# Kernel tuning notes

Measured on AMD Instinct MI355X. Metric: run time of the kernel, lower is better.

## Reference

```python
import jax, jax.numpy as jnp
import numpy as np

N_NODES = 50000
N_EDGES = 600000
BAG = 16
VOCAB = 10000
EMB = 128
HID = 128
N_CLASSES = 10
N_GRAPHS = 512
PAD_IDX = 1


def setup_inputs() -> dict:
    key = jax.random.key(0)
    ks = jax.random.split(key, 12)
    x_tokens = jax.random.randint(ks[0], (N_NODES, BAG), 0, VOCAB)
    src = jax.random.randint(ks[1], (N_EDGES,), 0, N_NODES)
    dst = jax.random.randint(ks[2], (N_EDGES,), 0, N_NODES)
    edge_index = jnp.stack([src, dst])
    batch = jnp.sort(jax.random.randint(ks[3], (N_NODES,), 0, N_GRAPHS))
    # rows 0,1 are zero in the original (weights[2:] filled from pretrained vectors)
    emb_table = (jax.random.normal(ks[4], (VOCAB, EMB)) * 0.02).at[:2].set(0.0)
    s = 1.0 / np.sqrt(EMB)
    w1_l = jax.random.normal(ks[5], (HID, EMB)) * s
    b1 = jnp.zeros((HID,), jnp.float32)
    w1_r = jax.random.normal(ks[6], (HID, EMB)) * s
    w2_l = jax.random.normal(ks[7], (HID, HID)) * s
    b2 = jnp.zeros((HID,), jnp.float32)
    w2_r = jax.random.normal(ks[8], (HID, HID)) * s
    w_out = jax.random.normal(ks[9], (N_CLASSES, HID)) * s
    b_out = jnp.zeros((N_CLASSES,), jnp.float32)
    return {"x_tokens": x_tokens, "edge_index": edge_index, "batch": batch,
            "emb_table": emb_table, "w1_l": w1_l, "b1": b1, "w1_r": w1_r,
            "w2_l": w2_l, "b2": b2, "w2_r": w2_r, "w_out": w_out, "b_out": b_out}


def _embedding_bag_mean(tokens, table):
    # nn.EmbeddingBag mode='mean' with padding_idx: padding tokens excluded from mean
    emb = table[tokens]                                  # [N, BAG, D]
    mask = (tokens != PAD_IDX)[..., None].astype(table.dtype)
    total = jnp.sum(emb * mask, axis=1)                  # [N, D]
    cnt = jnp.clip(jnp.sum(mask, axis=1), 1.0)           # [N, 1]
    return total / cnt


def _sage_conv(x, src, dst, w_l, b_l, w_r):
    # PyG SAGEConv: lin_l(mean_{j in N(i)} x_j) + lin_r(x_i); lin_r has no bias
    n = x.shape[0]
    msg_sum = jax.ops.segment_sum(x[src], dst, num_segments=n)           # [N, D]
    deg = jax.ops.segment_sum(jnp.ones((src.shape[0], 1), x.dtype), dst,
                              num_segments=n)                             # [N, 1]
    aggr = msg_sum / jnp.clip(deg, 1.0)
    return aggr @ w_l.T + b_l + x @ w_r.T


def reference(x_tokens, edge_index, batch, emb_table, w1_l, b1, w1_r,
              w2_l, b2, w2_r, w_out, b_out):
    src, dst = edge_index[0], edge_index[1]
    x = _embedding_bag_mean(x_tokens, emb_table)                 # [N, EMB]
    x = jax.nn.relu(_sage_conv(x, src, dst, w1_l, b1, w1_r))     # [N, HID]
    x = jax.nn.relu(_sage_conv(x, src, dst, w2_l, b2, w2_r))     # [N, HID]
    # global_mean_pool over graph ids
    g_sum = jax.ops.segment_sum(x, batch, num_segments=N_GRAPHS)
    g_cnt = jax.ops.segment_sum(jnp.ones((x.shape[0], 1), x.dtype), batch,
                                num_segments=N_GRAPHS)
    g = g_sum / jnp.clip(g_cnt, 1.0)                             # [G, HID]
    return g @ w_out.T + b_out                                   # [G, C]
```

## Files before the change

kernel.cpp:

```cpp
#include <hip/hip_runtime.h>
#include <hip/hip_bf16.h>

#define NN 50000
#define NE 600000
#define BAG 16
#define EMB 128
#define HID 128
#define NC 10
#define NG 512
#define PAD_IDX 1
#define VOCAB 10000
#define SLOTS 64
#define TPAIRS (VOCAB * EMB / 2)
#define WPAIRS (4 * HID * EMB / 2)
#define EMVB (NN / 16)
#define NCH1 293
#define RANGES 125
#define RNODES 400
#define QCAP 6400
#define NTILES ((NN + 127) / 128)

typedef __attribute__((ext_vector_type(8))) short v8s;
typedef __attribute__((ext_vector_type(4))) float v4f;

__device__ __forceinline__ float bflo(unsigned u) { return __uint_as_float(u << 16); }
__device__ __forceinline__ float bfhi(unsigned u) { return __uint_as_float(u & 0xffff0000u); }
__device__ __forceinline__ unsigned short f2bf(float f) {
    unsigned u = __float_as_uint(f);
    return (unsigned short)((u + 0x7fffu + ((u >> 16) & 1u)) >> 16);
}
__device__ __forceinline__ void acc8(float* a, v8s v) {
    unsigned* u = (unsigned*)&v;
#pragma unroll
    for (int j = 0; j < 4; j++) {
        a[2 * j] += bflo(u[j]);
        a[2 * j + 1] += bfhi(u[j]);
    }
}

__global__ void k_conv(const float* __restrict__ t, unsigned short* __restrict__ tb,
                       const float* __restrict__ w1l, const float* __restrict__ w1r,
                       const float* __restrict__ w2l, const float* __restrict__ w2r,
                       unsigned short* __restrict__ wbf, int* __restrict__ qtail,
                       float* __restrict__ gsum, float* __restrict__ gcnt,
                       unsigned short* __restrict__ x0, unsigned short* __restrict__ x1) {
    int i = blockIdx.x * blockDim.x + threadIdx.x;
    if (i < RANGES) qtail[i] = 0;
    if (i < NG * HID) gsum[i] = 0.f;
    if (i < NG) gcnt[i] = 0.f;
    if (i < 64) {
        ((unsigned*)(x0 + (size_t)NN * EMB))[i] = 0;
        ((unsigned*)(x1 + (size_t)NN * HID))[i] = 0;
    }
    if (i < TPAIRS) {
        float2 v = *(const float2*)(t + (size_t)i * 2);
        unsigned lo = f2bf(v.x), hi = f2bf(v.y);
        *(unsigned*)(tb + (size_t)i * 2) = lo | (hi << 16);
    } else if (i < TPAIRS + WPAIRS) {
        int j = i - TPAIRS;
        int k = j * 2;
        int arr = k >> 14;
        int o = k & 16383;
        const float* w = (arr == 0) ? w1l : (arr == 1) ? w1r : (arr == 2) ? w2l : w2r;
        float2 v = *(const float2*)(w + o);
        unsigned lo = f2bf(v.x), hi = f2bf(v.y);
        *(unsigned*)(wbf + k) = lo | (hi << 16);
    }
}

__global__ __launch_bounds__(256) void k_scatem(const int* __restrict__ src,
                                                const int* __restrict__ dst,
                                                int* __restrict__ qtail,
                                                unsigned* __restrict__ queue,
                                                const int* __restrict__ tokens,
                                                const unsigned short* __restrict__ table,
                                                unsigned short* __restrict__ x0) {
    __shared__ int qcntL[RANGES];
    __shared__ unsigned qbufL[RANGES * 64];
    int b = blockIdx.x;
    int tid = threadIdx.x;

    if (b < NCH1) {
        for (int i = tid; i < RANGES; i += 256) qcntL[i] = 0;
        __syncthreads();
        int e0 = b * 2048 + tid * 8;
        if (e0 < NE) {
            int4 s0 = *((const int4*)(src + e0));
            int4 s1 = *((const int4*)(src + e0) + 1);
            int4 d0 = *((const int4*)(dst + e0));
            int4 d1 = *((const int4*)(dst + e0) + 1);
            int ss[8] = {s0.x, s0.y, s0.z, s0.w, s1.x, s1.y, s1.z, s1.w};
            int dd[8] = {d0.x, d0.y, d0.z, d0.w, d1.x, d1.y, d1.z, d1.w};
#pragma unroll
            for (int j = 0; j < 8; j++) {
                int q = dd[j] / RNODES;
                unsigned pk = ((unsigned)(dd[j] - q * RNODES) << 16) | (unsigned)ss[j];
                int pos = atomicAdd(&qcntL[q], 1);
                if (pos < 64) qbufL[q * 64 + pos] = pk;
            }
        }
        __syncthreads();
        if (tid < RANGES) {
            int n = qcntL[tid];
            if (n > 64) n = 64;
            int base = atomicAdd(&qtail[tid], n);
            if (base + n > QCAP) n = (QCAP - base > 0) ? QCAP - base : 0;
            unsigned* qp = queue + (size_t)tid * QCAP + base;
            for (int k = 0; k < n; k++) qp[k] = qbufL[tid * 64 + k];
        }
        return;
    }

    int sl = tid & 15;
    int node = (b - NCH1) * 16 + (tid >> 4);
    const int* tp = tokens + node * BAG;
    int tk[16];
    *(int4*)(tk) = *(const int4*)(tp);
    *(int4*)(tk + 4) = *(const int4*)(tp + 4);
    *(int4*)(tk + 8) = *(const int4*)(tp + 8);
    *(int4*)(tk + 12) = *(const int4*)(tp + 12);
    int c = 0;
#pragma unroll
    for (int t = 0; t < BAG; t++) c += (tk[t] != PAD_IDX);
    float a[8];
#pragma unroll
    for (int j = 0; j < 8; j++) a[j] = 0.f;
#pragma unroll
    for (int h = 0; h < 2; h++) {
        v8s v[8];
#pragma unroll
        for (int t = 0; t < 8; t++)
            v[t] = *(const v8s*)(table + (size_t)tk[h * 8 + t] * EMB + sl * 8);
#pragma unroll
        for (int t = 0; t < 8; t++) acc8(a, v[t]);
    }
    float inv = 1.0f / (float)(c > 0 ? c : 1);
    uint4 o;
    o.x = f2bf(a[0] * inv) | ((unsigned)f2bf(a[1] * inv) << 16);
    o.y = f2bf(a[2] * inv) | ((unsigned)f2bf(a[3] * inv) << 16);
    o.z = f2bf(a[4] * inv) | ((unsigned)f2bf(a[5] * inv) << 16);
    o.w = f2bf(a[6] * inv) | ((unsigned)f2bf(a[7] * inv) << 16);
    *(uint4*)(x0 + (size_t)node * EMB + sl * 8) = o;
}

__global__ __launch_bounds__(256) void k_csr(const int* __restrict__ qtail,
                                             const unsigned* __restrict__ queue,
                                             int* __restrict__ cnt,
                                             unsigned short* __restrict__ slots) {
    __shared__ int cntL[RNODES];
    __shared__ __align__(16) unsigned short slotsL[RNODES * SLOTS];
    int r = blockIdx.x, tid = threadIdx.x;
    for (int i = tid; i < RNODES; i += 256) cntL[i] = 0;
    __syncthreads();
    int n = qtail[r];
    if (n > QCAP) n = QCAP;
    const unsigned* qp = queue + (size_t)r * QCAP;
    for (int i = tid; i < n; i += 256) {
        unsigned u = qp[i];
        int dl = u >> 16;
        int p = atomicAdd(&cntL[dl], 1);
        if (p < SLOTS) slotsL[dl * SLOTS + p] = (unsigned short)(u & 0xffffu);
    }
    __syncthreads();
    for (int i = tid; i < RNODES; i += 256) {
        int d = cntL[i];
        if (d > SLOTS) d = SLOTS;
        int d8 = (d + 7) & ~7;
        if (d8 > SLOTS) d8 = SLOTS;
        for (int p = d; p < d8; p++) slotsL[i * SLOTS + p] = (unsigned short)NN;
    }
    __syncthreads();
    uint4* gs = (uint4*)(slots + (size_t)r * RNODES * SLOTS);
    const uint4* ls = (const uint4*)slotsL;
    for (int i = tid; i < RNODES * SLOTS / 8; i += 256) gs[i] = ls[i];
    for (int i = tid; i < RNODES; i += 256) cnt[r * RNODES + i] = cntL[i];
}

__global__ __launch_bounds__(256) void k_aggr(const unsigned short* __restrict__ x,
                                              const int* __restrict__ cnt,
                                              const unsigned short* __restrict__ slots,
                                              unsigned short* __restrict__ aggr) {
    int wv = threadIdx.x >> 6;
    int lane = threadIdx.x & 63;
    int n0 = (blockIdx.x * 4 + wv) * 2;
    int n1 = n0 + 1;
    int g = lane >> 4, sl = lane & 15;
    int deg0 = cnt[n0], deg1 = cnt[n1];
    int m0 = deg0 > SLOTS ? SLOTS : deg0;
    int m1 = deg1 > SLOTS ? SLOTS : deg1;
    int m80 = (m0 + 7) & ~7;
    int m81 = (m1 + 7) & ~7;
    int idx0 = slots[(size_t)n0 * SLOTS + lane];
    int idx1 = slots[(size_t)n1 * SLOTS + lane];
    float a0[8], a1[8];
#pragma unroll
    for (int j = 0; j < 8; j++) {
        a0[j] = 0.f;
        a1[j] = 0.f;
    }
    int mm = m80 > m81 ? m80 : m81;
#pragma unroll 2
    for (int i = 0; i < mm; i += 8) {
        bool c0 = (i < m80), c1 = (i < m81);
        v8s w0, w1, w2, w3;
        if (c0) {
            int t00 = __shfl(idx0, i + g, 64);
            int t01 = __shfl(idx0, i + 4 + g, 64);
            w0 = *(const v8s*)(x + (size_t)t00 * HID + sl * 8);
            w1 = *(const v8s*)(x + (size_t)t01 * HID + sl * 8);
        }
        if (c1) {
            int t10 = __shfl(idx1, i + g, 64);
            int t11 = __shfl(idx1, i + 4 + g, 64);
            w2 = *(const v8s*)(x + (size_t)t10 * HID + sl * 8);
            w3 = *(const v8s*)(x + (size_t)t11 * HID + sl * 8);
        }
        if (c0) {
            acc8(a0, w0);
            acc8(a0, w1);
        }
        if (c1) {
            acc8(a1, w2);
            acc8(a1, w3);
        }
    }
#pragma unroll
    for (int j = 0; j < 8; j++) {
        a0[j] += __shfl_xor(a0[j], 16, 64);
        a0[j] += __shfl_xor(a0[j], 32, 64);
        a1[j] += __shfl_xor(a1[j], 16, 64);
        a1[j] += __shfl_xor(a1[j], 32, 64);
    }
    if (g == 0) {
        float inv = 1.0f / (float)(deg0 > 0 ? deg0 : 1);
        uint4 o;
        o.x = f2bf(a0[0] * inv) | ((unsigned)f2bf(a0[1] * inv) << 16);
        o.y = f2bf(a0[2] * inv) | ((unsigned)f2bf(a0[3] * inv) << 16);
        o.z = f2bf(a0[4] * inv) | ((unsigned)f2bf(a0[5] * inv) << 16);
        o.w = f2bf(a0[6] * inv) | ((unsigned)f2bf(a0[7] * inv) << 16);
        *(uint4*)(aggr + (size_t)n0 * HID + sl * 8) = o;
    } else if (g == 1) {
        float inv = 1.0f / (float)(deg1 > 0 ? deg1 : 1);
        uint4 o;
        o.x = f2bf(a1[0] * inv) | ((unsigned)f2bf(a1[1] * inv) << 16);
        o.y = f2bf(a1[2] * inv) | ((unsigned)f2bf(a1[3] * inv) << 16);
        o.z = f2bf(a1[4] * inv) | ((unsigned)f2bf(a1[5] * inv) << 16);
        o.w = f2bf(a1[6] * inv) | ((unsigned)f2bf(a1[7] * inv) << 16);
        *(uint4*)(aggr + (size_t)n1 * HID + sl * 8) = o;
    }
}

__device__ __forceinline__ void sage_kloop(int row0, const unsigned short* __restrict__ xa,
                                           const unsigned short* __restrict__ xr,
                                           const unsigned short* __restrict__ wl,
                                           const unsigned short* __restrict__ wr,
                                           unsigned short* As, unsigned short* Bs,
                                           v4f acc[2][8]) {
    int tid = threadIdx.x;
    int wave = tid >> 6, lane = tid & 63;
    int q = lane >> 4, l16 = lane & 15;
    for (int kc = 0; kc < 8; kc++) {
        const unsigned short* Ag = (kc < 4) ? xa : xr;
        const unsigned short* Bg = (kc < 4) ? wl : wr;
        int koff = (kc & 3) * 32;
#pragma unroll
        for (int it = 0; it < 2; it++) {
            int seg = tid + it * 256;
            int r = seg >> 2, sg = seg & 3;
            int gr = row0 + r;
            if (gr > NN - 1) gr = NN - 1;
            v8s a = *(const v8s*)(Ag + (size_t)gr * HID + koff + sg * 8);
            *(v8s*)(As + r * 32 + sg * 8) = a;
            v8s b = *(const v8s*)(Bg + (size_t)r * HID + koff + sg * 8);
            *(v8s*)(Bs + r * 32 + sg * 8) = b;
        }
        __syncthreads();
        v8s a0 = *(const v8s*)(As + (wave * 32 + l16) * 32 + q * 8);
        v8s a1 = *(const v8s*)(As + (wave * 32 + 16 + l16) * 32 + q * 8);
#pragma unroll
        for (int nt = 0; nt < 8; nt++) {
            v8s b = *(const v8s*)(Bs + (nt * 16 + l16) * 32 + q * 8);
            acc[0][nt] = __builtin_amdgcn_mfma_f32_16x16x32_bf16(a0, b, acc[0][nt], 0, 0, 0);
            acc[1][nt] = __builtin_amdgcn_mfma_f32_16x16x32_bf16(a1, b, acc[1][nt], 0, 0, 0);
        }
        __syncthreads();
    }
}

__global__ __launch_bounds__(256) void k_sage(const unsigned short* __restrict__ xa,
                                              const unsigned short* __restrict__ xr,
                                              const unsigned short* __restrict__ wl,
                                              const unsigned short* __restrict__ wr,
                                              const float* __restrict__ bias,
                                              unsigned short* __restrict__ out) {
    __shared__ unsigned short As[128 * 32];
    __shared__ unsigned short Bs[128 * 32];
    int row0 = blockIdx.x * 128;
    v4f acc[2][8];
#pragma unroll
    for (int m = 0; m < 2; m++)
#pragma unroll
        for (int n = 0; n < 8; n++) acc[m][n] = (v4f){0.f, 0.f, 0.f, 0.f};
    sage_kloop(row0, xa, xr, wl, wr, As, Bs, acc);
    int tid = threadIdx.x;
    int wave = tid >> 6, lane = tid & 63;
    int q = lane >> 4, l16 = lane & 15;
#pragma unroll
    for (int nt = 0; nt < 8; nt++) {
        int col = nt * 16 + l16;
        float bv = bias[col];
#pragma unroll
        for (int mt = 0; mt < 2; mt++) {
#pragma unroll
            for (int r = 0; r < 4; r++) {
                int row = row0 + wave * 32 + mt * 16 + q * 4 + r;
                if (row < NN) {
                    float v = acc[mt][nt][r] + bv;
                    v = v > 0.f ? v : 0.f;
                    out[(size_t)row * HID + col] = f2bf(v);
                }
            }
        }
    }
}

__global__ __launch_bounds__(256) void k_sagepool(const unsigned short* __restrict__ xa,
                                                  const unsigned short* __restrict__ xr,
                                                  const unsigned short* __restrict__ wl,
                                                  const unsigned short* __restrict__ wr,
                                                  const float* __restrict__ bias,
                                                  const int* __restrict__ batch,
                                                  float* __restrict__ gsum,
                                                  float* __restrict__ gcnt) {
    __shared__ unsigned short smem[128 * 128];
    unsigned short* As = smem;
    unsigned short* Bs = smem + 128 * 32;
    int row0 = blockIdx.x * 128;
    v4f acc[2][8];
#pragma unroll
    for (int m = 0; m < 2; m++)
#pragma unroll
        for (int n = 0; n < 8; n++) acc[m][n] = (v4f){0.f, 0.f, 0.f, 0.f};
    sage_kloop(row0, xa, xr, wl, wr, As, Bs, acc);
    int tid = threadIdx.x;
    int wave = tid >> 6, lane = tid & 63;
    int q = lane >> 4, l16 = lane & 15;
#pragma unroll
    for (int nt = 0; nt < 8; nt++) {
        int col = nt * 16 + l16;
        float bv = bias[col];
#pragma unroll
        for (int mt = 0; mt < 2; mt++) {
#pragma unroll
            for (int r = 0; r < 4; r++) {
                int rl = wave * 32 + mt * 16 + q * 4 + r;
                float v = acc[mt][nt][r] + bv;
                v = v > 0.f ? v : 0.f;
                smem[rl * 128 + col] = f2bf(v);
            }
        }
    }
    __syncthreads();
    if (tid < 128) {
        int col = tid;
        int end = NN - row0;
        if (end > 128) end = 128;
        int cur = batch[row0];
        float acc_p = 0.f;
        int c = 0;
        for (int i = 0; i < end; i++) {
            int b = batch[row0 + i];
            if (b != cur) {
                atomicAdd(&gsum[cur * HID + col], acc_p);
                if (col == 0) atomicAdd(&gcnt[cur], (float)c);
                acc_p = 0.f;
                c = 0;
                cur = b;
            }
            acc_p += __uint_as_float(((unsigned)smem[i * 128 + col]) << 16);
            c++;
        }
        atomicAdd(&gsum[cur * HID + col], acc_p);
        if (col == 0) atomicAdd(&gcnt[cur], (float)c);
    }
}

__global__ __launch_bounds__(128) void k_final(const float* __restrict__ gsum,
                                               const float* __restrict__ gcnt,
                                               const float* __restrict__ w_out,
                                               const float* __restrict__ b_out,
                                               float* __restrict__ out) {
    __shared__ float mean[HID];
    int g = blockIdx.x, tid = threadIdx.x;
    mean[tid] = gsum[g * HID + tid] / fmaxf(gcnt[g], 1.0f);
    __syncthreads();
    if (tid < NC) {
        float s = b_out[tid];
#pragma unroll 16
        for (int d = 0; d < HID; d++) s += mean[d] * w_out[tid * HID + d];
        out[g * NC + tid] = s;
    }
}

extern "C" void kernel_launch(void* const* d_in, const int* in_sizes, int n_in,
                              void* d_out, int out_size, void* d_ws, size_t ws_size,
                              hipStream_t stream) {
    const int* x_tokens = (const int*)d_in[0];
    const int* edge = (const int*)d_in[1];
    const int* batch = (const int*)d_in[2];
    const float* emb_table = (const float*)d_in[3];
    const float* w1l = (const float*)d_in[4];
    const float* b1 = (const float*)d_in[5];
    const float* w1r = (const float*)d_in[6];
    const float* w2l = (const float*)d_in[7];
    const float* b2 = (const float*)d_in[8];
    const float* w2r = (const float*)d_in[9];
    const float* w_out = (const float*)d_in[10];
    const float* b_out = (const float*)d_in[11];
    float* out = (float*)d_out;

    char* ws = (char*)d_ws;
    size_t off = 0;
    auto alloc = [&](size_t bytes) {
        void* p = ws + off;
        off += (bytes + 255) & ~(size_t)255;
        return p;
    };
    int* cnt = (int*)alloc(NN * 4);
    unsigned short* slots = (unsigned short*)alloc((size_t)NN * SLOTS * 2);
    unsigned short* wbf = (unsigned short*)alloc(4 * HID * EMB * 2);
    float* gsum = (float*)alloc(NG * HID * 4);
    float* gcnt = (float*)alloc(NG * 4);
    unsigned short* x0 = (unsigned short*)alloc((size_t)(NN + 1) * EMB * 2);
    unsigned short* x1 = (unsigned short*)alloc((size_t)(NN + 1) * HID * 2);
    unsigned short* aggrb = (unsigned short*)alloc((size_t)NN * HID * 2);
    unsigned* queue = (unsigned*)alloc((size_t)RANGES * QCAP * 4);
    int* qtail = (int*)alloc(RANGES * 4);
    unsigned short* table_bf = x1;

    const int* srcp = edge;
    const int* dstp = edge + NE;

    k_conv<<<(TPAIRS + WPAIRS + 255) / 256, 256, 0, stream>>>(
        emb_table, table_bf, w1l, w1r, w2l, w2r, wbf, qtail, gsum, gcnt, x0, x1);
    k_scatem<<<NCH1 + EMVB, 256, 0, stream>>>(srcp, dstp, qtail, queue, x_tokens,
                                              table_bf, x0);
    k_csr<<<RANGES, 256, 0, stream>>>(qtail, queue, cnt, slots);
    k_aggr<<<NN / 8, 256, 0, stream>>>(x0, cnt, slots, aggrb);
    k_sage<<<NTILES, 256, 0, stream>>>(aggrb, x0, wbf, wbf + 16384, b1, x1);
    k_aggr<<<NN / 8, 256, 0, stream>>>(x1, cnt, slots, aggrb);
    k_sagepool<<<NTILES, 256, 0, stream>>>(aggrb, x1, wbf + 32768, wbf + 49152, b2,
                                           batch, gsum, gcnt);
    k_final<<<NG, 128, 0, stream>>>(gsum, gcnt, w_out, b_out, out);
}
```

Baseline: 198.0 us.

## Fuse edge bucketing into conversion kernel and CSR into embed kernel; pipeline GEMM loads

```diff
diff --git a/kernel.cpp b/kernel.cpp
--- a/kernel.cpp
+++ b/kernel.cpp
@@ -13,12 +13,14 @@
 #define SLOTS 64
 #define TPAIRS (VOCAB * EMB / 2)
 #define WPAIRS (4 * HID * EMB / 2)
-#define EMVB (NN / 16)
+#define CONVB ((TPAIRS + WPAIRS + 255) / 256)
 #define NCH1 293
 #define RANGES 125
 #define RNODES 400
-#define QCAP 6400
+#define CSRB (RANGES * 2)
+#define EMVB (NN / 16)
 #define NTILES ((NN + 127) / 128)
+#define ASTR 40
 
 typedef __attribute__((ext_vector_type(8))) short v8s;
 typedef __attribute__((ext_vector_type(4))) float v4f;
@@ -38,14 +40,55 @@
     }
 }
 
-__global__ void k_conv(const float* __restrict__ t, unsigned short* __restrict__ tb,
-                       const float* __restrict__ w1l, const float* __restrict__ w1r,
-                       const float* __restrict__ w2l, const float* __restrict__ w2r,
-                       unsigned short* __restrict__ wbf, int* __restrict__ qtail,
-                       float* __restrict__ gsum, float* __restrict__ gcnt,
-                       unsigned short* __restrict__ x0, unsigned short* __restrict__ x1) {
-    int i = blockIdx.x * blockDim.x + threadIdx.x;
-    if (i < RANGES) qtail[i] = 0;
+__global__ __launch_bounds__(256) void k_conv(const int* __restrict__ src,
+                                              const int* __restrict__ dst,
+                                              unsigned* __restrict__ queue,
+                                              int* __restrict__ qcntG,
+                                              const float* __restrict__ t,
+                                              unsigned short* __restrict__ tb,
+                                              const float* __restrict__ w1l,
+                                              const float* __restrict__ w1r,
+                                              const float* __restrict__ w2l,
+                                              const float* __restrict__ w2r,
+                                              unsigned short* __restrict__ wbf,
+                                              float* __restrict__ gsum,
+                                              float* __restrict__ gcnt,
+                                              unsigned short* __restrict__ x0,
+                                              unsigned short* __restrict__ x1) {
+    __shared__ int qcL[RANGES];
+    __shared__ unsigned qbL[RANGES * 64];
+    int b = blockIdx.x;
+    int tid = threadIdx.x;
+    if (b < NCH1) {
+        for (int i = tid; i < RANGES; i += 256) qcL[i] = 0;
+        __syncthreads();
+        int e0 = b * 2048 + tid * 8;
+        if (e0 < NE) {
+            int4 s0 = *((const int4*)(src + e0));
+            int4 s1 = *((const int4*)(src + e0) + 1);
+            int4 d0 = *((const int4*)(dst + e0));
+            int4 d1 = *((const int4*)(dst + e0) + 1);
+            int ss[8] = {s0.x, s0.y, s0.z, s0.w, s1.x, s1.y, s1.z, s1.w};
+            int dd[8] = {d0.x, d0.y, d0.z, d0.w, d1.x, d1.y, d1.z, d1.w};
+#pragma unroll
+            for (int j = 0; j < 8; j++) {
+                int q = dd[j] / RNODES;
+                unsigned pk = ((unsigned)(dd[j] - q * RNODES) << 16) | (unsigned)ss[j];
+                int pos = atomicAdd(&qcL[q], 1);
+                if (pos < 64) qbL[q * 64 + pos] = pk;
+            }
+        }
+        __syncthreads();
+        if (tid < RANGES) {
+            int n = qcL[tid];
+            if (n > 64) n = 64;
+            qcntG[tid * NCH1 + b] = n;
+            unsigned* qp = queue + ((size_t)tid * NCH1 + b) * 64;
+            for (int k = 0; k < n; k++) qp[k] = qbL[tid * 64 + k];
+        }
+        return;
+    }
+    int i = (b - NCH1) * 256 + tid;
     if (i < NG * HID) gsum[i] = 0.f;
     if (i < NG) gcnt[i] = 0.f;
     if (i < 64) {
@@ -68,51 +111,52 @@
     }
 }
 
-__global__ __launch_bounds__(256) void k_scatem(const int* __restrict__ src,
-                                                const int* __restrict__ dst,
-                                                int* __restrict__ qtail,
-                                                unsigned* __restrict__ queue,
+__global__ __launch_bounds__(256) void k_scatem(const int* __restrict__ qcntG,
+                                                const unsigned* __restrict__ queue,
+                                                int* __restrict__ cnt,
+                                                unsigned short* __restrict__ slots,
                                                 const int* __restrict__ tokens,
                                                 const unsigned short* __restrict__ table,
                                                 unsigned short* __restrict__ x0) {
-    __shared__ int qcntL[RANGES];
-    __shared__ unsigned qbufL[RANGES * 64];
+    __shared__ int cntL[200];
+    __shared__ __align__(16) unsigned short slotsL[200 * SLOTS];
     int b = blockIdx.x;
     int tid = threadIdx.x;
-
-    if (b < NCH1) {
-        for (int i = tid; i < RANGES; i += 256) qcntL[i] = 0;
-        __syncthreads();
-        int e0 = b * 2048 + tid * 8;
-        if (e0 < NE) {
-            int4 s0 = *((const int4*)(src + e0));
-            int4 s1 = *((const int4*)(src + e0) + 1);
-            int4 d0 = *((const int4*)(dst + e0));
-            int4 d1 = *((const int4*)(dst + e0) + 1);
-            int ss[8] = {s0.x, s0.y, s0.z, s0.w, s1.x, s1.y, s1.z, s1.w};
-            int dd[8] = {d0.x, d0.y, d0.z, d0.w, d1.x, d1.y, d1.z, d1.w};
-#pragma unroll
-            for (int j = 0; j < 8; j++) {
-                int q = dd[j] / RNODES;
-                unsigned pk = ((unsigned)(dd[j] - q * RNODES) << 16) | (unsigned)ss[j];
-                int pos = atomicAdd(&qcntL[q], 1);
-                if (pos < 64) qbufL[q * 64 + pos] = pk;
+    if (b < CSRB) {
+        int r = b >> 1, half = b & 1;
+        for (int i = tid; i < 200; i += 256) cntL[i] = 0;
+        __syncthreads();
+        int dlo = half * 200;
+        for (int c = tid; c < NCH1; c += 256) {
+            int n = qcntG[r * NCH1 + c];
+            const unsigned* qp = queue + ((size_t)r * NCH1 + c) * 64;
+            for (int k = 0; k < n; k++) {
+                unsigned u = qp[k];
+                int d2 = (int)(u >> 16) - dlo;
+                if ((unsigned)d2 < 200u) {
+                    int p = atomicAdd(&cntL[d2], 1);
+                    if (p < SLOTS) slotsL[d2 * SLOTS + p] = (unsigned short)(u & 0xffffu);
+                }
             }
         }
         __syncthreads();
-        if (tid < RANGES) {
-            int n = qcntL[tid];
-            if (n > 64) n = 64;
-            int base = atomicAdd(&qtail[tid], n);
-            if (base + n > QCAP) n = (QCAP - base > 0) ? QCAP - base : 0;
-            unsigned* qp = queue + (size_t)tid * QCAP + base;
-            for (int k = 0; k < n; k++) qp[k] = qbufL[tid * 64 + k];
-        }
+        for (int i = tid; i < 200; i += 256) {
+            int d = cntL[i];
+            if (d > SLOTS) d = SLOTS;
+            int d8 = (d + 7) & ~7;
+            if (d8 > SLOTS) d8 = SLOTS;
+            for (int p = d; p < d8; p++) slotsL[i * SLOTS + p] = (unsigned short)NN;
+        }
+        __syncthreads();
+        int nb = r * RNODES + half * 200;
+        uint4* gs = (uint4*)(slots + (size_t)nb * SLOTS);
+        const uint4* ls = (const uint4*)slotsL;
+        for (int i = tid; i < 200 * SLOTS / 8; i += 256) gs[i] = ls[i];
+        for (int i = tid; i < 200; i += 256) cnt[nb + i] = cntL[i];
         return;
     }
-
     int sl = tid & 15;
-    int node = (b - NCH1) * 16 + (tid >> 4);
+    int node = (b - CSRB) * 16 + (tid >> 4);
     const int* tp = tokens + node * BAG;
     int tk[16];
     *(int4*)(tk) = *(const int4*)(tp);
@@ -125,15 +169,12 @@
     float a[8];
 #pragma unroll
     for (int j = 0; j < 8; j++) a[j] = 0.f;
-#pragma unroll
-    for (int h = 0; h < 2; h++) {
-        v8s v[8];
-#pragma unroll
-        for (int t = 0; t < 8; t++)
-            v[t] = *(const v8s*)(table + (size_t)tk[h * 8 + t] * EMB + sl * 8);
-#pragma unroll
-        for (int t = 0; t < 8; t++) acc8(a, v[t]);
-    }
+    v8s v[16];
+#pragma unroll
+    for (int t = 0; t < 16; t++)
+        v[t] = *(const v8s*)(table + (size_t)tk[t] * EMB + sl * 8);
+#pragma unroll
+    for (int t = 0; t < 16; t++) acc8(a, v[t]);
     float inv = 1.0f / (float)(c > 0 ? c : 1);
     uint4 o;
     o.x = f2bf(a[0] * inv) | ((unsigned)f2bf(a[1] * inv) << 16);
@@ -141,39 +182,6 @@
     o.z = f2bf(a[4] * inv) | ((unsigned)f2bf(a[5] * inv) << 16);
     o.w = f2bf(a[6] * inv) | ((unsigned)f2bf(a[7] * inv) << 16);
     *(uint4*)(x0 + (size_t)node * EMB + sl * 8) = o;
-}
-
-__global__ __launch_bounds__(256) void k_csr(const int* __restrict__ qtail,
-                                             const unsigned* __restrict__ queue,
-                                             int* __restrict__ cnt,
-                                             unsigned short* __restrict__ slots) {
-    __shared__ int cntL[RNODES];
-    __shared__ __align__(16) unsigned short slotsL[RNODES * SLOTS];
-    int r = blockIdx.x, tid = threadIdx.x;
-    for (int i = tid; i < RNODES; i += 256) cntL[i] = 0;
-    __syncthreads();
-    int n = qtail[r];
-    if (n > QCAP) n = QCAP;
-    const unsigned* qp = queue + (size_t)r * QCAP;
-    for (int i = tid; i < n; i += 256) {
-        unsigned u = qp[i];
-        int dl = u >> 16;
-        int p = atomicAdd(&cntL[dl], 1);
-        if (p < SLOTS) slotsL[dl * SLOTS + p] = (unsigned short)(u & 0xffffu);
-    }
-    __syncthreads();
-    for (int i = tid; i < RNODES; i += 256) {
-        int d = cntL[i];
-        if (d > SLOTS) d = SLOTS;
-        int d8 = (d + 7) & ~7;
-        if (d8 > SLOTS) d8 = SLOTS;
-        for (int p = d; p < d8; p++) slotsL[i * SLOTS + p] = (unsigned short)NN;
-    }
-    __syncthreads();
-    uint4* gs = (uint4*)(slots + (size_t)r * RNODES * SLOTS);
-    const uint4* ls = (const uint4*)slotsL;
-    for (int i = tid; i < RNODES * SLOTS / 8; i += 256) gs[i] = ls[i];
-    for (int i = tid; i < RNODES; i += 256) cnt[r * RNODES + i] = cntL[i];
 }
 
 __global__ __launch_bounds__(256) void k_aggr(const unsigned short* __restrict__ x,
@@ -259,32 +267,43 @@
     int tid = threadIdx.x;
     int wave = tid >> 6, lane = tid & 63;
     int q = lane >> 4, l16 = lane & 15;
+    int r0 = tid >> 2, sg = tid & 3;
+    int r1 = (tid + 256) >> 2;
+    int gr0 = row0 + r0;
+    if (gr0 > NN - 1) gr0 = NN - 1;
+    int gr1 = row0 + r1;
+    if (gr1 > NN - 1) gr1 = NN - 1;
+    v8s ra0 = *(const v8s*)(xa + (size_t)gr0 * HID + sg * 8);
+    v8s ra1 = *(const v8s*)(xa + (size_t)gr1 * HID + sg * 8);
+    v8s rb0 = *(const v8s*)(wl + (size_t)r0 * HID + sg * 8);
+    v8s rb1 = *(const v8s*)(wl + (size_t)r1 * HID + sg * 8);
     for (int kc = 0; kc < 8; kc++) {
-        const unsigned short* Ag = (kc < 4) ? xa : xr;
-        const unsigned short* Bg = (kc < 4) ? wl : wr;
-        int koff = (kc & 3) * 32;
-#pragma unroll
-        for (int it = 0; it < 2; it++) {
-            int seg = tid + it * 256;
-            int r = seg >> 2, sg = seg & 3;
-            int gr = row0 + r;
-            if (gr > NN - 1) gr = NN - 1;
-            v8s a = *(const v8s*)(Ag + (size_t)gr * HID + koff + sg * 8);
-            *(v8s*)(As + r * 32 + sg * 8) = a;
-            v8s b = *(const v8s*)(Bg + (size_t)r * HID + koff + sg * 8);
-            *(v8s*)(Bs + r * 32 + sg * 8) = b;
-        }
-        __syncthreads();
-        v8s a0 = *(const v8s*)(As + (wave * 32 + l16) * 32 + q * 8);
-        v8s a1 = *(const v8s*)(As + (wave * 32 + 16 + l16) * 32 + q * 8);
+        __syncthreads();
+        *(v8s*)(As + r0 * ASTR + sg * 8) = ra0;
+        *(v8s*)(As + r1 * ASTR + sg * 8) = ra1;
+        *(v8s*)(Bs + r0 * ASTR + sg * 8) = rb0;
+        *(v8s*)(Bs + r1 * ASTR + sg * 8) = rb1;
+        __syncthreads();
+        if (kc < 7) {
+            int kn = kc + 1;
+            const unsigned short* Ag = (kn < 4) ? xa : xr;
+            const unsigned short* Bg = (kn < 4) ? wl : wr;
+            int koff = (kn & 3) * 32;
+            ra0 = *(const v8s*)(Ag + (size_t)gr0 * HID + koff + sg * 8);
+            ra1 = *(const v8s*)(Ag + (size_t)gr1 * HID + koff + sg * 8);
+            rb0 = *(const v8s*)(Bg + (size_t)r0 * HID + koff + sg * 8);
+            rb1 = *(const v8s*)(Bg + (size_t)r1 * HID + koff + sg * 8);
+        }
+        v8s a0 = *(const v8s*)(As + (wave * 32 + l16) * ASTR + q * 8);
+        v8s a1 = *(const v8s*)(As + (wave * 32 + 16 + l16) * ASTR + q * 8);
 #pragma unroll
         for (int nt = 0; nt < 8; nt++) {
-            v8s b = *(const v8s*)(Bs + (nt * 16 + l16) * 32 + q * 8);
+            v8s b = *(const v8s*)(Bs + (nt * 16 + l16) * ASTR + q * 8);
             acc[0][nt] = __builtin_amdgcn_mfma_f32_16x16x32_bf16(a0, b, acc[0][nt], 0, 0, 0);
             acc[1][nt] = __builtin_amdgcn_mfma_f32_16x16x32_bf16(a1, b, acc[1][nt], 0, 0, 0);
         }
-        __syncthreads();
-    }
+    }
+    __syncthreads();
 }
 
 __global__ __launch_bounds__(256) void k_sage(const unsigned short* __restrict__ xa,
@@ -293,8 +312,8 @@
                                               const unsigned short* __restrict__ wr,
                                               const float* __restrict__ bias,
                                               unsigned short* __restrict__ out) {
-    __shared__ unsigned short As[128 * 32];
-    __shared__ unsigned short Bs[128 * 32];
+    __shared__ unsigned short As[128 * ASTR];
+    __shared__ unsigned short Bs[128 * ASTR];
     int row0 = blockIdx.x * 128;
     v4f acc[2][8];
 #pragma unroll
@@ -334,7 +353,7 @@
                                                   float* __restrict__ gcnt) {
     __shared__ unsigned short smem[128 * 128];
     unsigned short* As = smem;
-    unsigned short* Bs = smem + 128 * 32;
+    unsigned short* Bs = smem + 128 * ASTR;
     int row0 = blockIdx.x * 128;
     v4f acc[2][8];
 #pragma unroll
@@ -434,18 +453,18 @@
     unsigned short* x0 = (unsigned short*)alloc((size_t)(NN + 1) * EMB * 2);
     unsigned short* x1 = (unsigned short*)alloc((size_t)(NN + 1) * HID * 2);
     unsigned short* aggrb = (unsigned short*)alloc((size_t)NN * HID * 2);
-    unsigned* queue = (unsigned*)alloc((size_t)RANGES * QCAP * 4);
-    int* qtail = (int*)alloc(RANGES * 4);
+    unsigned* queue = (unsigned*)alloc((size_t)RANGES * NCH1 * 64 * 4);
+    int* qcntG = (int*)alloc((size_t)RANGES * NCH1 * 4);
     unsigned short* table_bf = x1;
 
     const int* srcp = edge;
     const int* dstp = edge + NE;
 
-    k_conv<<<(TPAIRS + WPAIRS + 255) / 256, 256, 0, stream>>>(
-        emb_table, table_bf, w1l, w1r, w2l, w2r, wbf, qtail, gsum, gcnt, x0, x1);
-    k_scatem<<<NCH1 + EMVB, 256, 0, stream>>>(srcp, dstp, qtail, queue, x_tokens,
+    k_conv<<<NCH1 + CONVB, 256, 0, stream>>>(srcp, dstp, queue, qcntG, emb_table,
+                                             table_bf, w1l, w1r, w2l, w2r, wbf,
+                                             gsum, gcnt, x0, x1);
+    k_scatem<<<CSRB + EMVB, 256, 0, stream>>>(qcntG, queue, cnt, slots, x_tokens,
                                               table_bf, x0);
-    k_csr<<<RANGES, 256, 0, stream>>>(qtail, queue, cnt, slots);
     k_aggr<<<NN / 8, 256, 0, stream>>>(x0, cnt, slots, aggrb);
     k_sage<<<NTILES, 256, 0, stream>>>(aggrb, x0, wbf, wbf + 16384, b1, x1);
     k_aggr<<<NN / 8, 256, 0, stream>>>(x1, cnt, slots, aggrb);
```

Result: no change. 195.6 us (median of 2 runs) (-1.2%).
